# Kernel tuning notes

Hardware: AMD Instinct MI355X
Metric: run time of the kernel (lower is better)

## Reference

```python
import jax, jax.numpy as jnp
import numpy as np

Q_STEPS, Q_TOKENS = 16, 64
KV_STEPS, KV_TOKENS = 64, 64
WINDOW = 2
TOPK = 32
DIM = 512
BATCH = 8
NUM_CONTEXTS = 2


def build_local_mask(q_steps, q_tokens, kv_steps, kv_tokens, window):
    # centers: nearest kv step for each query step
    centers = np.round(np.linspace(0, kv_steps - 1, q_steps)).astype(np.int64)
    steps = np.arange(kv_steps)
    allowed = np.abs(steps[None, :] - centers[:, None]) <= window  # [q_steps, kv_steps]
    allowed = np.repeat(np.repeat(allowed, q_tokens, axis=0), kv_tokens, axis=1)
    return jnp.where(jnp.asarray(allowed), 0.0, -jnp.inf).astype(jnp.float32)


MASK = build_local_mask(Q_STEPS, Q_TOKENS, KV_STEPS, KV_TOKENS, WINDOW)


def setup_inputs() -> dict:
    key = jax.random.key(0)
    ks = jax.random.split(key, 12)
    s = 1.0 / np.sqrt(DIM)
    return {
        "query": jax.random.normal(ks[0], (BATCH, Q_STEPS, Q_TOKENS, DIM), jnp.float32),
        "source": jax.random.normal(ks[1], (BATCH, KV_STEPS, KV_TOKENS, DIM), jnp.float32),
        "ctx1": jax.random.normal(ks[2], (BATCH, DIM), jnp.float32),
        "ctx2": jax.random.normal(ks[3], (BATCH, DIM), jnp.float32),
        "Wq": jax.random.normal(ks[4], (DIM, DIM), jnp.float32) * s,
        "bq": jnp.zeros((DIM,), jnp.float32),
        "Wk": jax.random.normal(ks[5], (DIM, DIM), jnp.float32) * s,
        "bk": jnp.zeros((DIM,), jnp.float32),
        "Wv": jax.random.normal(ks[6], (DIM, DIM), jnp.float32) * s,
        "bv": jnp.zeros((DIM,), jnp.float32),
        "Wo": jax.random.normal(ks[7], (DIM, DIM), jnp.float32) * s,
        "bo": jnp.zeros((DIM,), jnp.float32),
        "Wc": jax.random.normal(ks[8], (NUM_CONTEXTS * DIM, 2 * DIM), jnp.float32) * s,
        "bc": jnp.zeros((2 * DIM,), jnp.float32),
    }


def reference(query, source, ctx1, ctx2, Wq, bq, Wk, bk, Wv, bv, Wo, bo, Wc, bc):
    B = query.shape[0]
    # CrossScaleCondition: fuse contexts -> per-batch FiLM params gamma, beta [B, dim]
    fused = jnp.concatenate([ctx1, ctx2], axis=-1)          # [B, num_contexts*dim]
    gb = fused @ Wc + bc                                     # [B, 2*dim]
    gamma, beta = jnp.split(gb, 2, axis=-1)

    q_flat = query.reshape(B, Q_STEPS * Q_TOKENS, DIM)       # [B, Lq, d]
    src_flat = source.reshape(B, KV_STEPS * KV_TOKENS, DIM)  # [B, Lkv, d]

    q_mod = q_flat * (1.0 + gamma[:, None, :]) + beta[:, None, :]
    q = q_mod @ Wq + bq
    k = src_flat @ Wk + bk
    v = src_flat @ Wv + bv

    scores = jnp.einsum('bqd,bkd->bqk', q, k) / jnp.sqrt(jnp.float32(DIM))
    scores = scores + MASK[None]                             # local window mask

    topk_scores, topk_idx = jax.lax.top_k(scores, TOPK)      # [B, Lq, k]
    selected_v = jax.vmap(lambda vb, ib: vb[ib])(v, topk_idx)  # [B, Lq, k, d]

    attn = jax.nn.softmax(topk_scores, axis=-1)
    out = jnp.einsum('bqk,bqkd->bqd', attn, selected_v)
    out = out @ Wo + bo
    return out.reshape(B, Q_STEPS, Q_TOKENS, DIM)
```

## Files before the change

kernel.cpp:

```cpp
#include <hip/hip_runtime.h>

#define NWIN 320
#define SCORE_SCALE 0.04419417382415922f

__constant__ int CENTERS[16] = {0,4,8,13,17,21,25,29,34,38,42,46,50,55,59,63};

typedef __attribute__((ext_vector_type(8))) short v8s;
typedef __attribute__((ext_vector_type(4))) float v4f;

__device__ __forceinline__ float bflo(unsigned u) { return __uint_as_float(u << 16); }
__device__ __forceinline__ float bfhi(unsigned u) { return __uint_as_float(u & 0xffff0000u); }
__device__ __forceinline__ float bf2f(unsigned short h) { return __uint_as_float(((unsigned)h) << 16); }
__device__ __forceinline__ unsigned short f2bf(float x) {
  unsigned u = __float_as_uint(x);
  unsigned r = 0x7fffu + ((u >> 16) & 1u);
  return (unsigned short)((u + r) >> 16);
}

__device__ __forceinline__ int t64_off(int r, int k) {
  return ((r & 31) << 7) + (((((r >> 5) << 2) | (k >> 3)) ^ (r & 7)) << 4) + ((k & 7) << 1);
}
__device__ __forceinline__ int frag_off(int r, int g) {
  return ((r & 31) << 7) + (((((r >> 5) << 2) | g) ^ (r & 7)) << 4);
}

__device__ __forceinline__ void gload_lds16(const void* g, void* l) {
  __builtin_amdgcn_global_load_lds((const __attribute__((address_space(1))) unsigned int*)g,
                                   (__attribute__((address_space(3))) unsigned int*)l, 16, 0, 0);
}

__device__ __forceinline__ void cvt8pair(float4 a, float4 b, uint4& hi4, uint4& lo4) {
  float v[8] = {a.x, a.y, a.z, a.w, b.x, b.y, b.z, b.w};
  unsigned short h[8], l[8];
  #pragma unroll
  for (int e = 0; e < 8; ++e) {
    h[e] = f2bf(v[e]);
    l[e] = f2bf(v[e] - bf2f(h[e]));
  }
  hi4.x = (unsigned)h[0] | ((unsigned)h[1] << 16);
  hi4.y = (unsigned)h[2] | ((unsigned)h[3] << 16);
  hi4.z = (unsigned)h[4] | ((unsigned)h[5] << 16);
  hi4.w = (unsigned)h[6] | ((unsigned)h[7] << 16);
  lo4.x = (unsigned)l[0] | ((unsigned)l[1] << 16);
  lo4.y = (unsigned)l[2] | ((unsigned)l[3] << 16);
  lo4.z = (unsigned)l[4] | ((unsigned)l[5] << 16);
  lo4.w = (unsigned)l[6] | ((unsigned)l[7] << 16);
}

__device__ __forceinline__ uint4 cvt8hi(float4 a, float4 b) {
  uint4 r;
  r.x = (unsigned)f2bf(a.x) | ((unsigned)f2bf(a.y) << 16);
  r.y = (unsigned)f2bf(a.z) | ((unsigned)f2bf(a.w) << 16);
  r.z = (unsigned)f2bf(b.x) | ((unsigned)f2bf(b.y) << 16);
  r.w = (unsigned)f2bf(b.z) | ((unsigned)f2bf(b.w) << 16);
  return r;
}

__device__ __forceinline__ uint2 cvt4(float4 a) {
  uint2 r;
  r.x = (unsigned)f2bf(a.x) | ((unsigned)f2bf(a.y) << 16);
  r.y = (unsigned)f2bf(a.z) | ((unsigned)f2bf(a.w) << 16);
  return r;
}

__global__ __launch_bounds__(256) void prep1_kernel(
    const float* __restrict__ ctx1, const float* __restrict__ ctx2,
    const float* __restrict__ Wc,  float* __restrict__ part,
    const float* __restrict__ Wk,  const float* __restrict__ bq, float* __restrict__ u,
    const float* __restrict__ Wq,
    unsigned short* __restrict__ Wqh, unsigned short* __restrict__ Wql,
    unsigned short* __restrict__ Wkh, unsigned short* __restrict__ Wkl,
    const float* __restrict__ Wv, const float* __restrict__ Wo,
    unsigned short* __restrict__ Wvt, unsigned short* __restrict__ Wot)
{
  __shared__ char img[32768];
  const int bid = blockIdx.x;
  const int tid = threadIdx.x;

  if (bid < 256) {
    const int b = bid >> 5, sl = (bid >> 2) & 7, jq = bid & 3;
    const int j = jq * 256 + tid;
    const int i0 = sl * 128;
    float acc = 0.f;
    #pragma unroll 4
    for (int t = 0; t < 128; ++t) {
      const int i = i0 + t;
      const float f = (i < 512) ? ctx1[b * 512 + i] : ctx2[b * 512 + i - 512];
      acc = fmaf(f, Wc[(size_t)i * 1024 + j], acc);
    }
    part[(b * 8 + sl) * 1024 + j] = acc;
  } else if (bid < 384) {
    const int d = (bid - 256) * 4 + (tid >> 6);
    const int lane = tid & 63;
    float4 a0 = *(const float4*)&Wk[(size_t)d * 512 + lane * 8];
    float4 a1 = *(const float4*)&Wk[(size_t)d * 512 + lane * 8 + 4];
    float4 c0 = *(const float4*)&bq[lane * 8];
    float4 c1 = *(const float4*)&bq[lane * 8 + 4];
    float s = a0.x*c0.x + a0.y*c0.y + a0.z*c0.z + a0.w*c0.w
            + a1.x*c1.x + a1.y*c1.y + a1.z*c1.z + a1.w*c1.w;
    #pragma unroll
    for (int off = 32; off > 0; off >>= 1) s += __shfl_xor(s, off, 64);
    if (lane == 0) u[d] = s * SCORE_SCALE;
  } else if (bid < 640) {
    const int b = bid - 384;
    const int mat = b >> 7;
    const float* Wsrc = mat ? Wk : Wq;
    unsigned short* Wh = mat ? Wkh : Wqh;
    unsigned short* Wl = mat ? Wkl : Wql;
    const size_t e0 = (((size_t)(b & 127) * 256) + tid) * 8;
    float4 x0 = *(const float4*)&Wsrc[e0];
    float4 x1 = *(const float4*)&Wsrc[e0 + 4];
    uint4 h4, l4;
    cvt8pair(x0, x1, h4, l4);
    *(uint4*)&Wh[e0] = h4;
    *(uint4*)&Wl[e0] = l4;
  } else {
    const int cb = bid - 640;
    const int ktile = cb & 15;
    const int mat   = cb >> 4;
    const float* W = mat ? Wo : Wv;
    unsigned short* Dt = mat ? Wot : Wvt;
    const int k  = tid >> 3;
    const int nt = tid & 7;
    #pragma unroll
    for (int e4 = 0; e4 < 16; ++e4) {
      float4 w = *(const float4*)&W[(size_t)(ktile * 32 + k) * 512 + nt * 64 + e4 * 4];
      float vv[4] = {w.x, w.y, w.z, w.w};
      #pragma unroll
      for (int c = 0; c < 4; ++c) {
        const int n = e4 * 4 + c;
        *(unsigned short*)(img + nt * 4096 + t64_off(n, k)) = f2bf(vv[c]);
      }
    }
    __syncthreads();
    const uint4* src = (const uint4*)img;
    uint4* dst = (uint4*)((char*)Dt + (size_t)ktile * 32768);
    for (int i = tid; i < 2048; i += 256) dst[i] = src[i];
  }
}

__global__ __launch_bounds__(256) void prep2_kernel(
    const unsigned short* __restrict__ Wqh, const unsigned short* __restrict__ Wql,
    const unsigned short* __restrict__ Wkh, const unsigned short* __restrict__ Wkl,
    unsigned short* __restrict__ Gt,
    const float* __restrict__ part, const float* __restrict__ bc,
    float* __restrict__ gb)
{
  const int bid = blockIdx.x;
  const int tid = threadIdx.x;

  if (bid < 256) {
    const int lane = tid & 63, l15 = lane & 15, g = lane >> 4;
    const int wave = tid >> 6;
    const int t  = (bid << 2) | wave;
    const int ti = t >> 5, tj = t & 31;
    const int ib = ti << 4, jb = tj << 4;
    const size_t arow = (size_t)(ib + l15) * 512 + (g << 3);
    const size_t brow = (size_t)(jb + l15) * 512 + (g << 3);

    v4f acc = (v4f){0.f, 0.f, 0.f, 0.f};
    #pragma unroll 4
    for (int kk = 0; kk < 16; ++kk) {
      const int kd = kk * 32;
      const v8s ah = *(const v8s*)&Wqh[arow + kd];
      const v8s al = *(const v8s*)&Wql[arow + kd];
      const v8s bh = *(const v8s*)&Wkh[brow + kd];
      const v8s bl = *(const v8s*)&Wkl[brow + kd];
      acc = __builtin_amdgcn_mfma_f32_16x16x32_bf16(ah, bh, acc, 0, 0, 0);
      acc = __builtin_amdgcn_mfma_f32_16x16x32_bf16(al, bh, acc, 0, 0, 0);
      acc = __builtin_amdgcn_mfma_f32_16x16x32_bf16(ah, bl, acc, 0, 0, 0);
    }
    #pragma unroll
    for (int k = 0; k < 4; ++k) {
      const int gi = ib + (g << 2) + k;
      const int gj = jb + l15;
      const float v = acc[k] * SCORE_SCALE;
      const unsigned short hi = f2bf(v);
      const unsigned short lo = f2bf(v - bf2f(hi));
      const int toff = t64_off(gj & 63, gi & 31);
      *(unsigned short*)((char*)Gt + ((size_t)((gi >> 5) * 8 + (gj >> 6)) << 12) + toff) = hi;
      *(unsigned short*)((char*)Gt + ((size_t)(((gi >> 5) + 16) * 8 + (gj >> 6)) << 12) + toff) = lo;
    }
  } else {
    const int rb = bid - 256;
    const int b = rb >> 2, jq = rb & 3;
    const int j = jq * 256 + tid;
    float acc = bc[j];
    #pragma unroll
    for (int sl = 0; sl < 8; ++sl) acc += part[(b * 8 + sl) * 1024 + j];
    gb[b * 1024 + j] = acc;
  }
}

__global__ __launch_bounds__(256) void proj_split(
    const float* __restrict__ A, const unsigned short* __restrict__ Bt,
    const float* __restrict__ bias, const float* __restrict__ gb,
    unsigned short* __restrict__ Qgt)
{
  __shared__ char smem[49152];
  char* const LAh = smem;
  char* const LAl = smem + 8192;
  char* const LBh = smem + 16384;
  char* const LBl = smem + 32768;

  const int tid  = threadIdx.x;
  const int lane = tid & 63, l15 = lane & 15, g = lane >> 4;
  const int wave = tid >> 6, wm = wave >> 1, wn = wave & 1;
  const int bid = blockIdx.x;
  const int xcd = bid & 7, idx = bid >> 3;
  const int mBlk = (idx & 15) | (xcd << 4);
  const int nBlk = idx >> 4;

  const int sr = tid >> 2;
  const int sq = tid & 3;
  const size_t arow = (size_t)(mBlk * 64 + sr) * 512 + sq * 8;
  const int gbbase = ((mBlk >> 4) * 1024) + sq * 8;
  const int awoff = t64_off(sr, sq * 8);

  int aoff[2], boff[4];
  #pragma unroll
  for (int fm = 0; fm < 2; ++fm) aoff[fm] = frag_off(wm * 32 + fm * 16 + l15, g);
  #pragma unroll
  for (int fn = 0; fn < 4; ++fn) {
    const int n = wn * 64 + fn * 16 + l15;
    boff[fn] = ((n >> 6) << 12) + frag_off(n & 63, g);
  }

  v4f acc[2][4];
  #pragma unroll
  for (int fm = 0; fm < 2; ++fm)
    #pragma unroll
    for (int fn = 0; fn < 4; ++fn) acc[fm][fn] = (v4f){0.f, 0.f, 0.f, 0.f};

  for (int tk = 0; tk < 8; ++tk) {
    const int kd = tk * 64;
    #pragma unroll
    for (int ks = 0; ks < 2; ++ks) {
      const int tk32 = tk * 2 + ks;
      const char* gsh = (const char*)Bt + ((size_t)(tk32 * 8 + nBlk * 2) << 12) + (size_t)tid * 16;
      const char* gsl = (const char*)Bt + ((size_t)((tk32 + 16) * 8 + nBlk * 2) << 12) + (size_t)tid * 16;
      #pragma unroll
      for (int i = 0; i < 2; ++i) {
        gload_lds16(gsh + i * 4096, LBh + ks * 8192 + (wave << 10) + i * 4096);
        gload_lds16(gsl + i * 4096, LBl + ks * 8192 + (wave << 10) + i * 4096);
      }
    }
    #pragma unroll
    for (int ks = 0; ks < 2; ++ks) {
      const int kds = kd + ks * 32;
      float4 x0 = *(const float4*)&A[arow + kds];
      float4 x1 = *(const float4*)&A[arow + kds + 4];
      float4 g0 = *(const float4*)&gb[gbbase + kds];
      float4 g1 = *(const float4*)&gb[gbbase + kds + 4];
      float4 b0 = *(const float4*)&gb[gbbase + 512 + kds];
      float4 b1 = *(const float4*)&gb[gbbase + 512 + kds + 4];
      x0.x = fmaf(x0.x, 1.f + g0.x, b0.x); x0.y = fmaf(x0.y, 1.f + g0.y, b0.y);
      x0.z = fmaf(x0.z, 1.f + g0.z, b0.z); x0.w = fmaf(x0.w, 1.f + g0.w, b0.w);
      x1.x = fmaf(x1.x, 1.f + g1.x, b1.x); x1.y = fmaf(x1.y, 1.f + g1.y, b1.y);
      x1.z = fmaf(x1.z, 1.f + g1.z, b1.z); x1.w = fmaf(x1.w, 1.f + g1.w, b1.w);
      uint4 hi4, lo4;
      cvt8pair(x0, x1, hi4, lo4);
      *(uint4*)(LAh + ks * 4096 + awoff) = hi4;
      *(uint4*)(LAl + ks * 4096 + awoff) = lo4;
    }
    __syncthreads();
    #pragma unroll
    for (int ks = 0; ks < 2; ++ks) {
      const v8s ah0 = *(const v8s*)(LAh + ks * 4096 + aoff[0]);
      const v8s ah1 = *(const v8s*)(LAh + ks * 4096 + aoff[1]);
      const v8s al0 = *(const v8s*)(LAl + ks * 4096 + aoff[0]);
      const v8s al1 = *(const v8s*)(LAl + ks * 4096 + aoff[1]);
      #pragma unroll
      for (int fn = 0; fn < 4; ++fn) {
        const v8s bh = *(const v8s*)(LBh + ks * 8192 + boff[fn]);
        const v8s bl = *(const v8s*)(LBl + ks * 8192 + boff[fn]);
        acc[0][fn] = __builtin_amdgcn_mfma_f32_16x16x32_bf16(ah0, bh, acc[0][fn], 0, 0, 0);
        acc[1][fn] = __builtin_amdgcn_mfma_f32_16x16x32_bf16(ah1, bh, acc[1][fn], 0, 0, 0);
        acc[0][fn] = __builtin_amdgcn_mfma_f32_16x16x32_bf16(al0, bh, acc[0][fn], 0, 0, 0);
        acc[1][fn] = __builtin_amdgcn_mfma_f32_16x16x32_bf16(al1, bh, acc[1][fn], 0, 0, 0);
        acc[0][fn] = __builtin_amdgcn_mfma_f32_16x16x32_bf16(ah0, bl, acc[0][fn], 0, 0, 0);
        acc[1][fn] = __builtin_amdgcn_mfma_f32_16x16x32_bf16(ah1, bl, acc[1][fn], 0, 0, 0);
      }
    }
    __syncthreads();
  }

  #pragma unroll
  for (int fn = 0; fn < 4; ++fn) {
    const int col = nBlk * 128 + wn * 64 + fn * 16 + l15;
    const float bv = bias[col];
    const int kt = col >> 5;
    const int kk = col & 31;
    #pragma unroll
    for (int fm = 0; fm < 2; ++fm) {
      const int r0 = wm * 32 + fm * 16 + g * 4;
      #pragma unroll
      for (int k = 0; k < 4; ++k) {
        const float vv = acc[fm][fn][k] + bv;
        const unsigned short hi = f2bf(vv);
        const unsigned short lo = f2bf(vv - bf2f(hi));
        const int toff = t64_off(r0 + k, kk);
        *(unsigned short*)((char*)Qgt + ((size_t)(kt * 128 + mBlk) << 12) + toff) = hi;
        *(unsigned short*)((char*)Qgt + ((size_t)((kt + 16) * 128 + mBlk) << 12) + toff) = lo;
      }
    }
  }
}

__global__ __launch_bounds__(512) void proj_v(
    const float* __restrict__ A, const unsigned short* __restrict__ Bt,
    const float* __restrict__ bias, unsigned short* __restrict__ Cb)
{
  __shared__ char smem[8192 + 65536];
  char* const LA = smem;
  char* const LB = smem + 8192;

  const int tid  = threadIdx.x;
  const int lane = tid & 63, l15 = lane & 15, g = lane >> 4;
  const int wave = tid >> 6, wm = wave >> 2, wn = wave & 3;
  const int mBlk = blockIdx.x;

  const int sr  = tid >> 3;
  const int sq4 = tid & 7;
  const size_t arow = (size_t)(mBlk * 64 + sr) * 512 + sq4 * 4;
  const int awoff = t64_off(sr, sq4 * 4);

  int aoff[2], boff[8];
  #pragma unroll
  for (int fm = 0; fm < 2; ++fm) aoff[fm] = frag_off(wm * 32 + fm * 16 + l15, g);
  #pragma unroll
  for (int fn = 0; fn < 8; ++fn) {
    const int n = wn * 128 + fn * 16 + l15;
    boff[fn] = ((n >> 6) << 12) + frag_off(n & 63, g);
  }

  v4f acc[2][8];
  #pragma unroll
  for (int fm = 0; fm < 2; ++fm)
    #pragma unroll
    for (int fn = 0; fn < 8; ++fn) acc[fm][fn] = (v4f){0.f, 0.f, 0.f, 0.f};

  for (int tk = 0; tk < 8; ++tk) {
    const int kd = tk * 64;
    #pragma unroll
    for (int ks = 0; ks < 2; ++ks) {
      const char* gs = (const char*)Bt + ((size_t)(tk * 2 + ks) << 15) + (wave << 12) + (lane << 4);
      char* ld = LB + (ks << 15) + (wave << 12);
      #pragma unroll
      for (int i = 0; i < 4; ++i) gload_lds16(gs + (i << 10), ld + (i << 10));
    }
    #pragma unroll
    for (int ks = 0; ks < 2; ++ks) {
      float4 x = *(const float4*)&A[arow + kd + ks * 32];
      *(uint2*)(LA + (ks << 12) + awoff) = cvt4(x);
    }
    __syncthreads();
    #pragma unroll
    for (int ks = 0; ks < 2; ++ks) {
      const v8s a0 = *(const v8s*)(LA + (ks << 12) + aoff[0]);
      const v8s a1 = *(const v8s*)(LA + (ks << 12) + aoff[1]);
      #pragma unroll
      for (int fn = 0; fn < 8; ++fn) {
        const v8s bb = *(const v8s*)(LB + (ks << 15) + boff[fn]);
        acc[0][fn] = __builtin_amdgcn_mfma_f32_16x16x32_bf16(a0, bb, acc[0][fn], 0, 0, 0);
        acc[1][fn] = __builtin_amdgcn_mfma_f32_16x16x32_bf16(a1, bb, acc[1][fn], 0, 0, 0);
      }
    }
    __syncthreads();
  }

  #pragma unroll
  for (int fn = 0; fn < 8; ++fn) {
    const int col = wn * 128 + fn * 16 + l15;
    const float bv = bias[col];
    #pragma unroll
    for (int fm = 0; fm < 2; ++fm) {
      const int r0 = mBlk * 64 + wm * 32 + fm * 16 + g * 4;
      #pragma unroll
      for (int k = 0; k < 4; ++k)
        Cb[(size_t)(r0 + k) * 512 + col] = f2bf(acc[fm][fn][k] + bv);
    }
  }
}

__global__ __launch_bounds__(256) void proj_o(
    const float* __restrict__ A, const unsigned short* __restrict__ Bt,
    const float* __restrict__ bias, float* __restrict__ Cf)
{
  __shared__ char smem[12288];
  char* const LA = smem;
  char* const LB = smem + 4096;

  const int tid  = threadIdx.x;
  const int lane = tid & 63, l15 = lane & 15, g = lane >> 4;
  const int wave = tid >> 6, wm = wave >> 1, wn = wave & 1;
  const int bid = blockIdx.x;
  const int xcd = bid & 7, idx = bid >> 3;
  const int mBlk = (idx & 15) | (xcd << 4);
  const int nBlk = idx >> 4;

  const int sr = tid >> 2;
  const int sq = tid & 3;
  const size_t arow = (size_t)(mBlk * 64 + sr) * 512 + sq * 8;
  const int awoff = t64_off(sr, sq * 8);

  int aoff[2], boff[4];
  #pragma unroll
  for (int fm = 0; fm < 2; ++fm) aoff[fm] = frag_off(wm * 32 + fm * 16 + l15, g);
  #pragma unroll
  for (int fn = 0; fn < 4; ++fn) {
    const int n = wn * 64 + fn * 16 + l15;
    boff[fn] = ((n >> 6) << 12) + frag_off(n & 63, g);
  }

  v4f acc[2][4];
  #pragma unroll
  for (int fm = 0; fm < 2; ++fm)
    #pragma unroll
    for (int fn = 0; fn < 4; ++fn) acc[fm][fn] = (v4f){0.f, 0.f, 0.f, 0.f};

  for (int tk = 0; tk < 16; ++tk) {
    const int kd = tk * 32;
    {
      const char* gs = (const char*)Bt + ((size_t)tk << 15) + ((size_t)nBlk << 13) + (size_t)tid * 16;
      #pragma unroll
      for (int i = 0; i < 2; ++i)
        gload_lds16(gs + i * 4096, LB + (wave << 10) + i * 4096);
    }
    {
      float4 x0 = *(const float4*)&A[arow + kd];
      float4 x1 = *(const float4*)&A[arow + kd + 4];
      *(uint4*)(LA + awoff) = cvt8hi(x0, x1);
    }
    __syncthreads();
    const v8s a0 = *(const v8s*)(LA + aoff[0]);
    const v8s a1 = *(const v8s*)(LA + aoff[1]);
    #pragma unroll
    for (int fn = 0; fn < 4; ++fn) {
      const v8s bb = *(const v8s*)(LB + boff[fn]);
      acc[0][fn] = __builtin_amdgcn_mfma_f32_16x16x32_bf16(a0, bb, acc[0][fn], 0, 0, 0);
      acc[1][fn] = __builtin_amdgcn_mfma_f32_16x16x32_bf16(a1, bb, acc[1][fn], 0, 0, 0);
    }
    __syncthreads();
  }

  #pragma unroll
  for (int fn = 0; fn < 4; ++fn) {
    const int col = nBlk * 128 + wn * 64 + fn * 16 + l15;
    const float bv = bias[col];
    #pragma unroll
    for (int fm = 0; fm < 2; ++fm) {
      const int r0 = mBlk * 64 + wm * 32 + fm * 16 + g * 4;
      #pragma unroll
      for (int k = 0; k < 4; ++k)
        Cf[(size_t)(r0 + k) * 512 + col] = acc[fm][fn][k] + bv;
    }
  }
}

__global__ __launch_bounds__(256) void scores_mfma(
    const unsigned short* __restrict__ Qgt, const float* __restrict__ SRC,
    float* __restrict__ S)
{
  const int bs = blockIdx.y;
  const int s = bs & 15, b = bs >> 4;
  const int c  = CENTERS[s];
  const int lo = (c - 2 > 0) ? c - 2 : 0;
  const int hi = (c + 2 < 63) ? c + 2 : 63;
  if ((int)blockIdx.x > hi - lo) return;

  __shared__ char smem[16384];
  char* const LAh = smem;
  char* const LAl = smem + 4096;
  char* const LBh = smem + 8192;
  char* const LBl = smem + 12288;

  const int tid = threadIdx.x;
  const int lane = tid & 63, l15 = lane & 15, g = lane >> 4;
  const int wave = tid >> 6, wm = wave >> 1, wn = wave & 1;
  const int kvrow0 = (b << 12) + ((lo + (int)blockIdx.x) << 6);
  const int qbase  = bs << 6;
  const int sr = tid >> 2, sq = tid & 3;
  const size_t krow = (size_t)(kvrow0 + sr) * 512 + sq * 8;
  const int awoff = t64_off(sr, sq * 8);

  int aoff[2], boff[2];
  #pragma unroll
  for (int f = 0; f < 2; ++f) {
    aoff[f] = frag_off(wm * 32 + f * 16 + l15, g);
    boff[f] = frag_off(wn * 32 + f * 16 + l15, g);
  }

  v4f acc[2][2];
  #pragma unroll
  for (int i = 0; i < 2; ++i)
    #pragma unroll
    for (int j = 0; j < 2; ++j) acc[i][j] = (v4f){0.f, 0.f, 0.f, 0.f};

  for (int tk = 0; tk < 16; ++tk) {
    const int kd = tk * 32;
    {
      const char* gah = (const char*)Qgt + ((size_t)(tk * 128 + bs) << 12) + (size_t)tid * 16;
      const char* gal = (const char*)Qgt + ((size_t)((tk + 16) * 128 + bs) << 12) + (size_t)tid * 16;
      gload_lds16(gah, LAh + (wave << 10));
      gload_lds16(gal, LAl + (wave << 10));
    }
    {
      float4 y0 = *(const float4*)&SRC[krow + kd];
      float4 y1 = *(const float4*)&SRC[krow + kd + 4];
      uint4 bhi, blo;
      cvt8pair(y0, y1, bhi, blo);
      *(uint4*)(LBh + awoff) = bhi;
      *(uint4*)(LBl + awoff) = blo;
    }
    __syncthreads();
    const v8s a0h = *(const v8s*)(LAh + aoff[0]);
    const v8s a1h = *(const v8s*)(LAh + aoff[1]);
    const v8s a0l = *(const v8s*)(LAl + aoff[0]);
    const v8s a1l = *(const v8s*)(LAl + aoff[1]);
    const v8s b0h = *(const v8s*)(LBh + boff[0]);
    const v8s b1h = *(const v8s*)(LBh + boff[1]);
    const v8s b0l = *(const v8s*)(LBl + boff[0]);
    const v8s b1l = *(const v8s*)(LBl + boff[1]);
    acc[0][0] = __builtin_amdgcn_mfma_f32_16x16x32_bf16(a0h, b0h, acc[0][0], 0, 0, 0);
    acc[0][1] = __builtin_amdgcn_mfma_f32_16x16x32_bf16(a0h, b1h, acc[0][1], 0, 0, 0);
    acc[1][0] = __builtin_amdgcn_mfma_f32_16x16x32_bf16(a1h, b0h, acc[1][0], 0, 0, 0);
    acc[1][1] = __builtin_amdgcn_mfma_f32_16x16x32_bf16(a1h, b1h, acc[1][1], 0, 0, 0);
    acc[0][0] = __builtin_amdgcn_mfma_f32_16x16x32_bf16(a0l, b0h, acc[0][0], 0, 0, 0);
    acc[0][1] = __builtin_amdgcn_mfma_f32_16x16x32_bf16(a0l, b1h, acc[0][1], 0, 0, 0);
    acc[1][0] = __builtin_amdgcn_mfma_f32_16x16x32_bf16(a1l, b0h, acc[1][0], 0, 0, 0);
    acc[1][1] = __builtin_amdgcn_mfma_f32_16x16x32_bf16(a1l, b1h, acc[1][1], 0, 0, 0);
    acc[0][0] = __builtin_amdgcn_mfma_f32_16x16x32_bf16(a0h, b0l, acc[0][0], 0, 0, 0);
    acc[0][1] = __builtin_amdgcn_mfma_f32_16x16x32_bf16(a0h, b1l, acc[0][1], 0, 0, 0);
    acc[1][0] = __builtin_amdgcn_mfma_f32_16x16x32_bf16(a1h, b0l, acc[1][0], 0, 0, 0);
    acc[1][1] = __builtin_amdgcn_mfma_f32_16x16x32_bf16(a1h, b1l, acc[1][1], 0, 0, 0);
    __syncthreads();
  }

  #pragma unroll
  for (int fn = 0; fn < 2; ++fn) {
    const int cl = wn * 32 + fn * 16 + l15;
    const int colS = ((int)blockIdx.x << 6) + cl;
    #pragma unroll
    for (int fm = 0; fm < 2; ++fm) {
      const int r0 = qbase + wm * 32 + fm * 16 + g * 4;
      #pragma unroll
      for (int k = 0; k < 4; ++k)
        S[(size_t)(r0 + k) * NWIN + colS] = acc[fm][fn][k];
    }
  }
}

__global__ __launch_bounds__(256) void topk_pv(
    const float* __restrict__ S, const unsigned short* __restrict__ Vb,
    float* __restrict__ O)
{
  __shared__ int   sel_i[4][32];
  __shared__ float sel_p[4][32];

  const int lane = threadIdx.x & 63;
  const int wv   = threadIdx.x >> 6;
  const int b0   = blockIdx.x;
  const int grp  = (b0 & 7) + ((b0 >> 7) << 3);
  const int blk  = (b0 >> 3) & 15;
  const int row  = (((grp << 4) + blk) << 2) + wv;
  const int b    = row >> 10;
  const int s    = (row >> 6) & 15;
  const int c    = CENTERS[s];
  const int lo   = (c - 2 > 0) ? c - 2 : 0;
  const int hi   = (c + 2 < 63) ? c + 2 : 63;
  const int L    = (hi - lo + 1) << 6;
  const size_t vbase = ((size_t)b << 12) + ((size_t)lo << 6);

  const float* srow = S + (size_t)row * NWIN;
  float f[5]; unsigned uo[5];
  #pragma unroll
  for (int j = 0; j < 5; ++j) {
    const int idx = lane + (j << 6);
    const float v = (idx < L) ? srow[idx] : -__builtin_inff();
    f[j] = v;
    const unsigned fb = __float_as_uint(v);
    uo[j] = (fb & 0x80000000u) ? ~fb : (fb | 0x80000000u);
  }

  float m = f[0];
  #pragma unroll
  for (int j = 1; j < 5; ++j) m = fmaxf(m, f[j]);
  #pragma unroll
  for (int off = 32; off > 0; off >>= 1) m = fmaxf(m, __shfl_xor(m, off, 64));

  unsigned T = 0u;
  for (int bit = 31; bit >= 0; --bit) {
    const unsigned cand = T | (1u << bit);
    int cnt = 0;
    #pragma unroll
    for (int j = 0; j < 5; ++j)
      cnt += __popcll(__ballot(uo[j] >= cand));
    if (cnt >= 32) T = cand;
  }

  int base = 0;
  #pragma unroll
  for (int j = 0; j < 5; ++j) {
    const unsigned long long gm = __ballot(uo[j] > T);
    if (uo[j] > T) {
      const int rank = base + __builtin_amdgcn_mbcnt_hi(
          (unsigned)(gm >> 32), __builtin_amdgcn_mbcnt_lo((unsigned)gm, 0));
      sel_i[wv][rank] = lane + (j << 6);
      sel_p[wv][rank] = __expf(f[j] - m);
    }
    base += __popcll(gm);
  }
  #pragma unroll
  for (int j = 0; j < 5; ++j) {
    const unsigned long long em = __ballot(uo[j] == T);
    if (uo[j] == T) {
      const int er = base + __builtin_amdgcn_mbcnt_hi(
          (unsigned)(em >> 32), __builtin_amdgcn_mbcnt_lo((unsigned)em, 0));
      if (er < 32) {
        sel_i[wv][er] = lane + (j << 6);
        sel_p[wv][er] = __expf(f[j] - m);
      }
    }
    base += __popcll(em);
  }

  asm volatile("s_waitcnt lgkmcnt(0)" ::: "memory");

  const int   si = sel_i[wv][lane & 31];
  const float sp = sel_p[wv][lane & 31];
  float dp = (lane < 32) ? sp : 0.f;
  #pragma unroll
  for (int off = 32; off > 0; off >>= 1) dp += __shfl_xor(dp, off, 64);

  float oacc[8] = {0.f,0.f,0.f,0.f,0.f,0.f,0.f,0.f};
  #pragma unroll
  for (int tb = 0; tb < 32; tb += 4) {
    unsigned raws[4][4];
    #pragma unroll
    for (int q = 0; q < 4; ++q) {
      const int idx_t = __builtin_amdgcn_readlane(si, tb + q);
      const unsigned short* vrow = Vb + ((vbase + (size_t)idx_t) << 9);
      #pragma unroll
      for (int e = 0; e < 4; ++e)
        raws[q][e] = *(const unsigned*)&vrow[(lane << 1) + (e << 7)];
    }
    #pragma unroll
    for (int q = 0; q < 4; ++q) {
      const float p_t = __uint_as_float(
          (unsigned)__builtin_amdgcn_readlane((int)__float_as_uint(sp), tb + q));
      #pragma unroll
      for (int e = 0; e < 4; ++e) {
        oacc[2*e]     = fmaf(p_t, bflo(raws[q][e]), oacc[2*e]);
        oacc[2*e + 1] = fmaf(p_t, bfhi(raws[q][e]), oacc[2*e + 1]);
      }
    }
  }

  const float inv = 1.0f / dp;
  float* orow = O + ((size_t)row << 9);
  #pragma unroll
  for (int e = 0; e < 4; ++e) {
    float2 o2 = make_float2(oacc[2*e] * inv, oacc[2*e + 1] * inv);
    *(float2*)&orow[(lane << 1) + (e << 7)] = o2;
  }
}

extern "C" void kernel_launch(void* const* d_in, const int* in_sizes, int n_in,
                              void* d_out, int out_size, void* d_ws, size_t ws_size,
                              hipStream_t stream)
{
  (void)in_sizes; (void)n_in; (void)out_size; (void)ws_size;

  const float* query  = (const float*)d_in[0];
  const float* source = (const float*)d_in[1];
  const float* ctx1   = (const float*)d_in[2];
  const float* ctx2   = (const float*)d_in[3];
  const float* Wq     = (const float*)d_in[4];
  const float* bq     = (const float*)d_in[5];
  const float* Wk     = (const float*)d_in[6];
  const float* Wv     = (const float*)d_in[8];
  const float* bv     = (const float*)d_in[9];
  const float* Wo     = (const float*)d_in[10];
  const float* bo     = (const float*)d_in[11];
  const float* Wc     = (const float*)d_in[12];
  const float* bc     = (const float*)d_in[13];
  float* out = (float*)d_out;

  char* ws = (char*)d_ws;
  unsigned short* Qgt  = (unsigned short*)(ws);
  unsigned short* v    = (unsigned short*)(ws + 16777216);
  float*          S    = (float*)(ws + 50331648);
  float*          ctx  = (float*)(ws + 60817408);
  unsigned short* Gt   = (unsigned short*)(ws + 77594624);
  unsigned short* Wvt  = (unsigned short*)(ws + 78643200);
  unsigned short* Wot  = (unsigned short*)(ws + 79167488);
  float*          gb   = (float*)(ws + 79691776);
  float*          part = (float*)(ws + 79724544);
  float*          u    = (float*)(ws + 79986688);
  unsigned short* Wqh  = (unsigned short*)(ws + 79988736);
  unsigned short* Wql  = (unsigned short*)(ws + 80513024);
  unsigned short* Wkh  = (unsigned short*)(ws + 81037312);
  unsigned short* Wkl  = (unsigned short*)(ws + 81561600);

  prep1_kernel<<<672, 256, 0, stream>>>(ctx1, ctx2, Wc, part, Wk, bq, u, Wq,
                                        Wqh, Wql, Wkh, Wkl, Wv, Wo, Wvt, Wot);
  prep2_kernel<<<288, 256, 0, stream>>>(Wqh, Wql, Wkh, Wkl, Gt, part, bc, gb);
  proj_split<<<512, 256, 0, stream>>>(query, Gt, u, gb, Qgt);
  proj_v<<<512, 512, 0, stream>>>(source, Wvt, bv, v);
  scores_mfma<<<dim3(5, 128), 256, 0, stream>>>(Qgt, source, S);
  topk_pv<<<2048, 256, 0, stream>>>(S, v, ctx);
  proj_o<<<512, 256, 0, stream>>>(ctx, Wot, bo, out);
}
```

Before: 146.0 us.

## Double-buffer LDS tiles in projection GEMMs to overlap loads with MFMA

Converts the proj_split, K/V projection and proj_o GEMM main loops to a two-stage LDS ping-pong. The next K-slice's B tile is issued as async global-to-LDS loads and the A tile is held in registers while MFMAs run on the current buffer, leaving one barrier per iteration. This hides global-load latency behind compute, at the cost of more LDS per block in proj_o and more live registers, which may reduce occupancy. In proj_split and the K/V projection the K step also shrinks from 64 to 32 per iteration, doubling the iteration count.

```diff
diff --git a/kernel.cpp b/kernel.cpp
--- a/kernel.cpp
+++ b/kernel.cpp
@@ -198,11 +198,6 @@
     unsigned short* __restrict__ Qgt)
 {
   __shared__ char smem[49152];
-  char* const LAh = smem;
-  char* const LAl = smem + 8192;
-  char* const LBh = smem + 16384;
-  char* const LBl = smem + 32768;
-
   const int tid  = threadIdx.x;
   const int lane = tid & 63, l15 = lane & 15, g = lane >> 4;
   const int wave = tid >> 6, wm = wave >> 1, wn = wave & 1;
@@ -232,56 +227,67 @@
     #pragma unroll
     for (int fn = 0; fn < 4; ++fn) acc[fm][fn] = (v4f){0.f, 0.f, 0.f, 0.f};
 
-  for (int tk = 0; tk < 8; ++tk) {
-    const int kd = tk * 64;
-    #pragma unroll
-    for (int ks = 0; ks < 2; ++ks) {
-      const int tk32 = tk * 2 + ks;
-      const char* gsh = (const char*)Bt + ((size_t)(tk32 * 8 + nBlk * 2) << 12) + (size_t)tid * 16;
-      const char* gsl = (const char*)Bt + ((size_t)((tk32 + 16) * 8 + nBlk * 2) << 12) + (size_t)tid * 16;
-      #pragma unroll
-      for (int i = 0; i < 2; ++i) {
-        gload_lds16(gsh + i * 4096, LBh + ks * 8192 + (wave << 10) + i * 4096);
-        gload_lds16(gsl + i * 4096, LBl + ks * 8192 + (wave << 10) + i * 4096);
-      }
-    }
-    #pragma unroll
-    for (int ks = 0; ks < 2; ++ks) {
-      const int kds = kd + ks * 32;
-      float4 x0 = *(const float4*)&A[arow + kds];
-      float4 x1 = *(const float4*)&A[arow + kds + 4];
-      float4 g0 = *(const float4*)&gb[gbbase + kds];
-      float4 g1 = *(const float4*)&gb[gbbase + kds + 4];
-      float4 b0 = *(const float4*)&gb[gbbase + 512 + kds];
-      float4 b1 = *(const float4*)&gb[gbbase + 512 + kds + 4];
-      x0.x = fmaf(x0.x, 1.f + g0.x, b0.x); x0.y = fmaf(x0.y, 1.f + g0.y, b0.y);
-      x0.z = fmaf(x0.z, 1.f + g0.z, b0.z); x0.w = fmaf(x0.w, 1.f + g0.w, b0.w);
-      x1.x = fmaf(x1.x, 1.f + g1.x, b1.x); x1.y = fmaf(x1.y, 1.f + g1.y, b1.y);
-      x1.z = fmaf(x1.z, 1.f + g1.z, b1.z); x1.w = fmaf(x1.w, 1.f + g1.w, b1.w);
-      uint4 hi4, lo4;
-      cvt8pair(x0, x1, hi4, lo4);
-      *(uint4*)(LAh + ks * 4096 + awoff) = hi4;
-      *(uint4*)(LAl + ks * 4096 + awoff) = lo4;
-    }
-    __syncthreads();
-    #pragma unroll
-    for (int ks = 0; ks < 2; ++ks) {
-      const v8s ah0 = *(const v8s*)(LAh + ks * 4096 + aoff[0]);
-      const v8s ah1 = *(const v8s*)(LAh + ks * 4096 + aoff[1]);
-      const v8s al0 = *(const v8s*)(LAl + ks * 4096 + aoff[0]);
-      const v8s al1 = *(const v8s*)(LAl + ks * 4096 + aoff[1]);
-      #pragma unroll
-      for (int fn = 0; fn < 4; ++fn) {
-        const v8s bh = *(const v8s*)(LBh + ks * 8192 + boff[fn]);
-        const v8s bl = *(const v8s*)(LBl + ks * 8192 + boff[fn]);
-        acc[0][fn] = __builtin_amdgcn_mfma_f32_16x16x32_bf16(ah0, bh, acc[0][fn], 0, 0, 0);
-        acc[1][fn] = __builtin_amdgcn_mfma_f32_16x16x32_bf16(ah1, bh, acc[1][fn], 0, 0, 0);
-        acc[0][fn] = __builtin_amdgcn_mfma_f32_16x16x32_bf16(al0, bh, acc[0][fn], 0, 0, 0);
-        acc[1][fn] = __builtin_amdgcn_mfma_f32_16x16x32_bf16(al1, bh, acc[1][fn], 0, 0, 0);
-        acc[0][fn] = __builtin_amdgcn_mfma_f32_16x16x32_bf16(ah0, bl, acc[0][fn], 0, 0, 0);
-        acc[1][fn] = __builtin_amdgcn_mfma_f32_16x16x32_bf16(ah1, bl, acc[1][fn], 0, 0, 0);
-      }
-    }
+  auto stageB = [&](int buf, int tk) {
+    const char* gsh = (const char*)Bt + ((size_t)(tk * 8 + nBlk * 2) << 12) + (size_t)tid * 16;
+    const char* gsl = (const char*)Bt + ((size_t)((tk + 16) * 8 + nBlk * 2) << 12) + (size_t)tid * 16;
+    char* dh = smem + buf * 24576 + 8192 + (wave << 10);
+    char* dl = smem + buf * 24576 + 16384 + (wave << 10);
+    #pragma unroll
+    for (int i = 0; i < 2; ++i) {
+      gload_lds16(gsh + i * 4096, dh + i * 4096);
+      gload_lds16(gsl + i * 4096, dl + i * 4096);
+    }
+  };
+  auto loadA = [&](int tk, float4* r) {
+    const int kd = tk * 32;
+    r[0] = *(const float4*)&A[arow + kd];
+    r[1] = *(const float4*)&A[arow + kd + 4];
+    r[2] = *(const float4*)&gb[gbbase + kd];
+    r[3] = *(const float4*)&gb[gbbase + kd + 4];
+    r[4] = *(const float4*)&gb[gbbase + 512 + kd];
+    r[5] = *(const float4*)&gb[gbbase + 512 + kd + 4];
+  };
+  auto writeA = [&](int buf, float4* r) {
+    float4 x0 = r[0], x1 = r[1];
+    x0.x = fmaf(x0.x, 1.f + r[2].x, r[4].x); x0.y = fmaf(x0.y, 1.f + r[2].y, r[4].y);
+    x0.z = fmaf(x0.z, 1.f + r[2].z, r[4].z); x0.w = fmaf(x0.w, 1.f + r[2].w, r[4].w);
+    x1.x = fmaf(x1.x, 1.f + r[3].x, r[5].x); x1.y = fmaf(x1.y, 1.f + r[3].y, r[5].y);
+    x1.z = fmaf(x1.z, 1.f + r[3].z, r[5].z); x1.w = fmaf(x1.w, 1.f + r[3].w, r[5].w);
+    uint4 hi4, lo4;
+    cvt8pair(x0, x1, hi4, lo4);
+    *(uint4*)(smem + buf * 24576 + awoff) = hi4;
+    *(uint4*)(smem + buf * 24576 + 4096 + awoff) = lo4;
+  };
+
+  float4 pr[6];
+  stageB(0, 0);
+  loadA(0, pr);
+  writeA(0, pr);
+  __syncthreads();
+
+  for (int tk = 0; tk < 16; ++tk) {
+    const int cur = tk & 1;
+    if (tk < 15) {
+      stageB(cur ^ 1, tk + 1);
+      loadA(tk + 1, pr);
+    }
+    const char* base = smem + cur * 24576;
+    const v8s ah0 = *(const v8s*)(base + aoff[0]);
+    const v8s ah1 = *(const v8s*)(base + aoff[1]);
+    const v8s al0 = *(const v8s*)(base + 4096 + aoff[0]);
+    const v8s al1 = *(const v8s*)(base + 4096 + aoff[1]);
+    #pragma unroll
+    for (int fn = 0; fn < 4; ++fn) {
+      const v8s bh = *(const v8s*)(base + 8192 + boff[fn]);
+      const v8s bl = *(const v8s*)(base + 16384 + boff[fn]);
+      acc[0][fn] = __builtin_amdgcn_mfma_f32_16x16x32_bf16(ah0, bh, acc[0][fn], 0, 0, 0);
+      acc[1][fn] = __builtin_amdgcn_mfma_f32_16x16x32_bf16(ah1, bh, acc[1][fn], 0, 0, 0);
+      acc[0][fn] = __builtin_amdgcn_mfma_f32_16x16x32_bf16(al0, bh, acc[0][fn], 0, 0, 0);
+      acc[1][fn] = __builtin_amdgcn_mfma_f32_16x16x32_bf16(al1, bh, acc[1][fn], 0, 0, 0);
+      acc[0][fn] = __builtin_amdgcn_mfma_f32_16x16x32_bf16(ah0, bl, acc[0][fn], 0, 0, 0);
+      acc[1][fn] = __builtin_amdgcn_mfma_f32_16x16x32_bf16(ah1, bl, acc[1][fn], 0, 0, 0);
+    }
+    if (tk < 15) writeA(cur ^ 1, pr);
     __syncthreads();
   }
 
@@ -340,32 +346,33 @@
     #pragma unroll
     for (int fn = 0; fn < 8; ++fn) acc[fm][fn] = (v4f){0.f, 0.f, 0.f, 0.f};
 
-  for (int tk = 0; tk < 8; ++tk) {
-    const int kd = tk * 64;
-    #pragma unroll
-    for (int ks = 0; ks < 2; ++ks) {
-      const char* gs = (const char*)Bt + ((size_t)(tk * 2 + ks) << 15) + (wave << 12) + (lane << 4);
-      char* ld = LB + (ks << 15) + (wave << 12);
-      #pragma unroll
-      for (int i = 0; i < 4; ++i) gload_lds16(gs + (i << 10), ld + (i << 10));
-    }
-    #pragma unroll
-    for (int ks = 0; ks < 2; ++ks) {
-      float4 x = *(const float4*)&A[arow + kd + ks * 32];
-      *(uint2*)(LA + (ks << 12) + awoff) = cvt4(x);
-    }
-    __syncthreads();
-    #pragma unroll
-    for (int ks = 0; ks < 2; ++ks) {
-      const v8s a0 = *(const v8s*)(LA + (ks << 12) + aoff[0]);
-      const v8s a1 = *(const v8s*)(LA + (ks << 12) + aoff[1]);
-      #pragma unroll
-      for (int fn = 0; fn < 8; ++fn) {
-        const v8s bb = *(const v8s*)(LB + (ks << 15) + boff[fn]);
-        acc[0][fn] = __builtin_amdgcn_mfma_f32_16x16x32_bf16(a0, bb, acc[0][fn], 0, 0, 0);
-        acc[1][fn] = __builtin_amdgcn_mfma_f32_16x16x32_bf16(a1, bb, acc[1][fn], 0, 0, 0);
-      }
-    }
+  auto stageB = [&](int buf, int tk) {
+    const char* gs = (const char*)Bt + ((size_t)tk << 15) + (wave << 12) + (lane << 4);
+    char* ld = LB + (buf << 15) + (wave << 12);
+    #pragma unroll
+    for (int i = 0; i < 4; ++i) gload_lds16(gs + (i << 10), ld + (i << 10));
+  };
+
+  float4 xa = *(const float4*)&A[arow];
+  stageB(0, 0);
+  *(uint2*)(LA + awoff) = cvt4(xa);
+  __syncthreads();
+
+  for (int tk = 0; tk < 16; ++tk) {
+    const int cur = tk & 1;
+    if (tk < 15) {
+      stageB(cur ^ 1, tk + 1);
+      xa = *(const float4*)&A[arow + (tk + 1) * 32];
+    }
+    const v8s a0 = *(const v8s*)(LA + (cur << 12) + aoff[0]);
+    const v8s a1 = *(const v8s*)(LA + (cur << 12) + aoff[1]);
+    #pragma unroll
+    for (int fn = 0; fn < 8; ++fn) {
+      const v8s bb = *(const v8s*)(LB + (cur << 15) + boff[fn]);
+      acc[0][fn] = __builtin_amdgcn_mfma_f32_16x16x32_bf16(a0, bb, acc[0][fn], 0, 0, 0);
+      acc[1][fn] = __builtin_amdgcn_mfma_f32_16x16x32_bf16(a1, bb, acc[1][fn], 0, 0, 0);
+    }
+    if (tk < 15) *(uint2*)(LA + ((cur ^ 1) << 12) + awoff) = cvt4(xa);
     __syncthreads();
   }
 
@@ -387,10 +394,7 @@
     const float* __restrict__ A, const unsigned short* __restrict__ Bt,
     const float* __restrict__ bias, float* __restrict__ Cf)
 {
-  __shared__ char smem[12288];
-  char* const LA = smem;
-  char* const LB = smem + 4096;
-
+  __shared__ char smem[24576];
   const int tid  = threadIdx.x;
   const int lane = tid & 63, l15 = lane & 15, g = lane >> 4;
   const int wave = tid >> 6, wm = wave >> 1, wn = wave & 1;
@@ -419,28 +423,37 @@
     #pragma unroll
     for (int fn = 0; fn < 4; ++fn) acc[fm][fn] = (v4f){0.f, 0.f, 0.f, 0.f};
 
+  auto stageB = [&](int buf, int tk) {
+    const char* gs = (const char*)Bt + ((size_t)tk << 15) + ((size_t)nBlk << 13) + (size_t)tid * 16;
+    char* ld = smem + buf * 12288 + 4096 + (wave << 10);
+    #pragma unroll
+    for (int i = 0; i < 2; ++i)
+      gload_lds16(gs + i * 4096, ld + i * 4096);
+  };
+
+  float4 x0 = *(const float4*)&A[arow];
+  float4 x1 = *(const float4*)&A[arow + 4];
+  stageB(0, 0);
+  *(uint4*)(smem + awoff) = cvt8hi(x0, x1);
+  __syncthreads();
+
   for (int tk = 0; tk < 16; ++tk) {
-    const int kd = tk * 32;
-    {
-      const char* gs = (const char*)Bt + ((size_t)tk << 15) + ((size_t)nBlk << 13) + (size_t)tid * 16;
-      #pragma unroll
-      for (int i = 0; i < 2; ++i)
-        gload_lds16(gs + i * 4096, LB + (wave << 10) + i * 4096);
-    }
-    {
-      float4 x0 = *(const float4*)&A[arow + kd];
-      float4 x1 = *(const float4*)&A[arow + kd + 4];
-      *(uint4*)(LA + awoff) = cvt8hi(x0, x1);
-    }
-    __syncthreads();
-    const v8s a0 = *(const v8s*)(LA + aoff[0]);
-    const v8s a1 = *(const v8s*)(LA + aoff[1]);
+    const int cur = tk & 1;
+    if (tk < 15) {
+      stageB(cur ^ 1, tk + 1);
+      x0 = *(const float4*)&A[arow + (tk + 1) * 32];
+      x1 = *(const float4*)&A[arow + (tk + 1) * 32 + 4];
+    }
+    const char* base = smem + cur * 12288;
+    const v8s a0 = *(const v8s*)(base + aoff[0]);
+    const v8s a1 = *(const v8s*)(base + aoff[1]);
     #pragma unroll
     for (int fn = 0; fn < 4; ++fn) {
-      const v8s bb = *(const v8s*)(LB + boff[fn]);
+      const v8s bb = *(const v8s*)(base + 4096 + boff[fn]);
       acc[0][fn] = __builtin_amdgcn_mfma_f32_16x16x32_bf16(a0, bb, acc[0][fn], 0, 0, 0);
       acc[1][fn] = __builtin_amdgcn_mfma_f32_16x16x32_bf16(a1, bb, acc[1][fn], 0, 0, 0);
     }
+    if (tk < 15) *(uint4*)(smem + (cur ^ 1) * 12288 + awoff) = cvt8hi(x0, x1);
     __syncthreads();
   }
 
```

New measurement: 142.4 us. 2.5% less time.
